# Optimization experiments

Hardware: AMD Instinct MI355X
Metric: run time of the kernel (lower is better)

Reference implementation:

```python
import jax, jax.numpy as jnp
import numpy as np

DEPTH = 10
HID = 48
IN_DIM = 784
OUT_DIM = 10
STEPS = 20
LR = 0.1
BATCH = 65536


def setup_inputs() -> dict:
    key = jax.random.key(0)
    ks = jax.random.split(key, 8)
    x = jax.random.normal(ks[0], (BATCH, IN_DIM), dtype=jnp.float32)
    target = jax.random.randint(ks[1], (BATCH,), 0, OUT_DIM)
    W0 = jax.random.normal(ks[2], (HID, IN_DIM), dtype=jnp.float32) / np.sqrt(IN_DIM)
    b0 = jnp.zeros((HID,), dtype=jnp.float32)
    Wh = jax.random.normal(ks[3], (DEPTH - 1, HID, HID), dtype=jnp.float32) / np.sqrt(HID)
    bh = jnp.zeros((DEPTH - 1, HID), dtype=jnp.float32)
    Wout = jax.random.normal(ks[4], (OUT_DIM, HID), dtype=jnp.float32) / np.sqrt(HID)
    bout = jnp.zeros((OUT_DIM,), dtype=jnp.float32)
    return {"x": x, "target": target, "W0": W0, "b0": b0, "Wh": Wh, "bh": bh, "Wout": Wout, "bout": bout}


def _settle(x, target, W0, b0, Wh, bh, Wout, bout):
    # hidden-layer weights: weights[0] = (W0,b0); weights[i] = (Wh[i-1],bh[i-1]) for 1<=i<DEPTH;
    # output layer weights[DEPTH] = (Wout,bout)
    def hw(i):
        return (W0, b0) if i == 0 else (Wh[i - 1], bh[i - 1])

    # init value nodes with a standard forward pass
    vals = []
    h = x
    for i in range(DEPTH):
        Wi, bi = hw(i)
        h = jax.nn.relu(h @ Wi.T + bi)
        vals.append(h)
    V = jnp.stack(vals, 0)  # (DEPTH, B, HID) = v_1..v_DEPTH
    v_out = jax.nn.one_hot(target, OUT_DIM, dtype=jnp.float32)  # clamped output v_{DEPTH+1}

    def step(V, _):
        vs = [x] + [V[i] for i in range(DEPTH)] + [v_out]
        # prediction errors (computed once per settling step, from pre-step values)
        errors = []
        for i in range(DEPTH):
            Wi, bi = hw(i)
            pre = vs[i] @ Wi.T + bi
            errors.append(vs[i + 1] - jax.nn.relu(pre))
        errors.append(vs[DEPTH + 1] - (vs[DEPTH] @ Wout.T + bout))
        # value-node updates: dE/dv_i = eps_{i-1} - J_i^T eps_i
        new = []
        for i in range(1, DEPTH + 1):
            bu = errors[i - 1]
            if i < DEPTH:
                Wi, bi = hw(i)
                pre = vs[i] @ Wi.T + bi
                td = (errors[i] * (pre > 0).astype(pre.dtype)) @ Wi
            else:
                td = errors[DEPTH] @ Wout
            vi = vs[i] - LR * (bu - td)
            new.append(jnp.clip(vi, -10.0, 10.0))
        return jnp.stack(new, 0), None

    V, _ = jax.lax.scan(step, V, None, length=STEPS)
    return V  # (DEPTH, B, HID): settled hidden value nodes v_1..v_DEPTH


def reference(x, target, W0, b0, Wh, bh, Wout, bout):
    return _settle(x, target, W0, b0, Wh, bh, Wout, bout)
```

## Files before the change

### kernel.cpp

```cpp
#include <hip/hip_runtime.h>
#include <stdint.h>

typedef __attribute__((ext_vector_type(4))) _Float16 half4;
typedef __attribute__((ext_vector_type(2))) _Float16 h2;
typedef __attribute__((ext_vector_type(4))) float f32x4;
typedef __attribute__((ext_vector_type(2))) uint32_t uint2v;
typedef __attribute__((ext_vector_type(2))) short short2v;

#define BLOCK 256
#define MFMA16 __builtin_amdgcn_mfma_f32_16x16x16f16
#define SCHEDB __builtin_amdgcn_sched_barrier
#define PKRTZ  __builtin_amdgcn_cvt_pkrtz

#define TD_OFF    41472
#define BH_OFF    59904
#define LDS_BYTES 61632

extern __shared__ unsigned char smem[];

#define B32H(X) __builtin_bit_cast(uint32_t, (X))
#define H2U(X)  __builtin_bit_cast(h2, (X))

#define PACK4(S0,S1,S2,S3) __extension__({ \
  half4 _b; \
  _b[0] = (_Float16)(S0); _b[1] = (_Float16)(S1); \
  _b[2] = (_Float16)(S2); _b[3] = (_Float16)(S3); \
  _b; })
#define PACKU(S0,S1) __extension__({ \
  h2 _x; _x[0] = (_Float16)(S0); _x[1] = (_Float16)(S1); B32H(_x); })

#define VB(ROW, KS) __extension__({ \
  uint2v _u; _u[0] = (ROW)[2*(KS)]; _u[1] = (ROW)[2*(KS)+1]; \
  __builtin_bit_cast(half4, _u); })

#define TDA(I, ST) ((I) <= 5 \
  ? tdreg[(I) <= 5 ? (I)-1 : 0][ST] \
  : *(const half4*)(smem + TD_OFF + ((I) >= 6 ? (I)-6 : 0)*4608 + (ST)*512 + lane*8))

#define PRED48(SRCU, WOFF, LIDX, P0, P1, P2) do { \
  P0 = *(const f32x4*)(smem + BH_OFF + ((LIDX)*48 +  0)*4 + b*16); \
  P1 = *(const f32x4*)(smem + BH_OFF + ((LIDX)*48 + 16)*4 + b*16); \
  P2 = *(const f32x4*)(smem + BH_OFF + ((LIDX)*48 + 32)*4 + b*16); \
  _Pragma("unroll") \
  for (int _ks = 0; _ks < 3; ++_ks) { \
    half4 _B = VB(SRCU, _ks); \
    half4 _A0 = *(const half4*)(smem + (WOFF) + (0*3+_ks)*512 + lane*8); \
    half4 _A1 = *(const half4*)(smem + (WOFF) + (1*3+_ks)*512 + lane*8); \
    half4 _A2 = *(const half4*)(smem + (WOFF) + (2*3+_ks)*512 + lane*8); \
    P0 = MFMA16(_A0, _B, P0, 0, 0, 0); \
    P1 = MFMA16(_A1, _B, P1, 0, 0, 0); \
    P2 = MFMA16(_A2, _B, P2, 0, 0, 0); \
  } \
} while(0)

#define TD48(MEU, I, T0, T1, T2) do { \
  T0 = (f32x4){0.f,0.f,0.f,0.f}; T1 = T0; T2 = T0; \
  _Pragma("unroll") \
  for (int _ks = 0; _ks < 3; ++_ks) { \
    half4 _B = VB(MEU, _ks); \
    half4 _A0 = TDA(I, 0*3+_ks); \
    half4 _A1 = TDA(I, 1*3+_ks); \
    half4 _A2 = TDA(I, 2*3+_ks); \
    T0 = MFMA16(_A0, _B, T0, 0, 0, 0); \
    T1 = MFMA16(_A1, _B, T1, 0, 0, 0); \
    T2 = MFMA16(_A2, _B, T2, 0, 0, 0); \
  } \
} while(0)

#define PREP2(PLO, PHI, VU32, ERRU, MEU) do { \
  uint32_t _p = B32H(PKRTZ((PLO), (PHI))); \
  uint32_t _sm = __builtin_bit_cast(uint32_t, \
      (short2v)(__builtin_bit_cast(short2v, _p) >> 15)); \
  uint32_t _nsm = ~_sm; \
  uint32_t _rl = _p & _nsm; \
  h2 _e = H2U(VU32) - H2U(_rl); \
  ERRU = B32H(_e); \
  MEU = ERRU & _nsm; \
} while(0)

#define UPD2(TLO, THI, EPKU, VU, ERRU) do { \
  uint32_t _t = B32H(PKRTZ((TLO), (THI))); \
  h2 _d = H2U(EPKU) - H2U(_t); \
  h2 _nv = H2U(VU) - HLR2*_d; \
  _nv = __builtin_elementwise_min(__builtin_elementwise_max(_nv, NCLP2), PCLP2); \
  VU = B32H(_nv); \
  EPKU = ERRU; \
} while(0)

#define LAYER_STEP(I) do { \
  f32x4 _p0, _p1, _p2; \
  PRED48(vhu[(I)-1], ((I)-1)*4608, (I)-1, _p0, _p1, _p2); \
  uint32_t _err[6], _me[6]; \
  PREP2(_p0[0], _p0[1], vhu[I][0], _err[0], _me[0]); \
  PREP2(_p0[2], _p0[3], vhu[I][1], _err[1], _me[1]); \
  PREP2(_p1[0], _p1[1], vhu[I][2], _err[2], _me[2]); \
  PREP2(_p1[2], _p1[3], vhu[I][3], _err[3], _me[3]); \
  PREP2(_p2[0], _p2[1], vhu[I][4], _err[4], _me[4]); \
  PREP2(_p2[2], _p2[3], vhu[I][5], _err[5], _me[5]); \
  f32x4 _t0, _t1, _t2; \
  TD48(_me, I, _t0, _t1, _t2); \
  UPD2(_t0[0], _t0[1], epku[0], vhu[(I)-1][0], _err[0]); \
  UPD2(_t0[2], _t0[3], epku[1], vhu[(I)-1][1], _err[1]); \
  UPD2(_t1[0], _t1[1], epku[2], vhu[(I)-1][2], _err[2]); \
  UPD2(_t1[2], _t1[3], epku[3], vhu[(I)-1][3], _err[3]); \
  UPD2(_t2[0], _t2[1], epku[4], vhu[(I)-1][4], _err[4]); \
  UPD2(_t2[2], _t2[3], epku[5], vhu[(I)-1][5], _err[5]); \
} while(0)

#define FWD(I) do { \
  f32x4 _p0, _p1, _p2; \
  PRED48(vhu[(I)-1], ((I)-1)*4608, (I)-1, _p0, _p1, _p2); \
  vhu[I][0] = PACKU(fmaxf(_p0[0],0.f), fmaxf(_p0[1],0.f)); \
  vhu[I][1] = PACKU(fmaxf(_p0[2],0.f), fmaxf(_p0[3],0.f)); \
  vhu[I][2] = PACKU(fmaxf(_p1[0],0.f), fmaxf(_p1[1],0.f)); \
  vhu[I][3] = PACKU(fmaxf(_p1[2],0.f), fmaxf(_p1[3],0.f)); \
  vhu[I][4] = PACKU(fmaxf(_p2[0],0.f), fmaxf(_p2[1],0.f)); \
  vhu[I][5] = PACKU(fmaxf(_p2[2],0.f), fmaxf(_p2[3],0.f)); \
} while(0)

__global__ __launch_bounds__(BLOCK) __attribute__((amdgpu_waves_per_eu(1, 2)))
void pcnet_kernel(const float* __restrict__ x, const int* __restrict__ target,
                  const float* __restrict__ W0, const float* __restrict__ b0,
                  const float* __restrict__ Wh, const float* __restrict__ bh,
                  const float* __restrict__ Wout, const float* __restrict__ bout,
                  float* __restrict__ out)
{
    const int t = threadIdx.x;
    const int lane = t & 63;
    const int wv = t >> 6;
    const int n = lane & 15;
    const int b = lane >> 4;

    const int bsamp0 = blockIdx.x*64 + wv*16;
    const int samp = bsamp0 + n;

    const h2 HLR2  = (h2)(_Float16)0.1f;
    const h2 PCLP2 = (h2)(_Float16)10.0f;
    const h2 NCLP2 = (h2)(_Float16)(-10.0f);

    f32x4 acc0[3];
    #pragma unroll
    for (int tm = 0; tm < 3; ++tm) acc0[tm] = (f32x4){0.f, 0.f, 0.f, 0.f};

    const float* xrow = x + (size_t)samp*784;
    for (int ch = 0; ch < 7; ++ch) {
        __syncthreads();
        for (int idx = t; idx < 1344; idx += BLOCK) {
            int st = idx >> 6, LB = idx & 63;
            int tm = st / 7, ksl = st - tm*7;
            int row = 16*tm + (LB & 15);
            int col = ch*112 + ksl*16 + 4*(LB >> 4);
            float4 w4 = *(const float4*)(W0 + row*784 + col);
            *(half4*)(smem + (tm*7+ksl)*512 + LB*8) = PACK4(w4.x, w4.y, w4.z, w4.w);
        }
        __syncthreads();
        #pragma unroll
        for (int ksl = 0; ksl < 7; ++ksl) {
            float4 xv = *(const float4*)(xrow + ch*112 + ksl*16 + 4*b);
            half4 xb = PACK4(xv.x, xv.y, xv.z, xv.w);
            #pragma unroll
            for (int tm = 0; tm < 3; ++tm) {
                half4 A = *(const half4*)(smem + (tm*7+ksl)*512 + lane*8);
                acc0[tm] = MFMA16(A, xb, acc0[tm], 0, 0, 0);
            }
        }
    }

    uint32_t vhu[10][6], a0u[6];
    #pragma unroll
    for (int tm = 0; tm < 3; ++tm) {
        float4 bb = *(const float4*)(b0 + 16*tm + 4*b);
        uint32_t lo = PACKU(fmaxf(acc0[tm][0] + bb.x, 0.f), fmaxf(acc0[tm][1] + bb.y, 0.f));
        uint32_t hi = PACKU(fmaxf(acc0[tm][2] + bb.z, 0.f), fmaxf(acc0[tm][3] + bb.w, 0.f));
        a0u[2*tm] = lo;   vhu[0][2*tm] = lo;
        a0u[2*tm+1] = hi; vhu[0][2*tm+1] = hi;
    }
    __syncthreads();

    for (int idx = t; idx < 5184; idx += BLOCK) {
        int L = idx / 576;
        int r2 = idx - L*576;
        int st = r2 >> 6, LB = r2 & 63;
        int tm = st / 3, ks = st - tm*3;
        int m  = 16*tm + (LB & 15);
        int k0 = 16*ks + 4*(LB >> 4);
        float4 w4 = *(const float4*)(Wh + L*2304 + m*48 + k0);
        *(half4*)(smem + L*4608 + st*512 + LB*8) = PACK4(w4.x, w4.y, w4.z, w4.w);
    }
    for (int idx = t; idx < 2304; idx += BLOCK) {
        int Lt = idx / 576;
        int r2 = idx - Lt*576;
        int st = r2 >> 6, LB = r2 & 63;
        int tm = st / 3, ks = st - tm*3;
        int m  = 16*tm + (LB & 15);
        int k0 = 16*ks + 4*(LB >> 4);
        const float* p = Wh + (Lt+5)*2304 + k0*48 + m;
        *(half4*)(smem + TD_OFF + Lt*4608 + st*512 + LB*8) = PACK4(p[0], p[48], p[96], p[144]);
    }
    for (int idx = t; idx < 432; idx += BLOCK)
        *(float*)(smem + BH_OFF + idx*4) = bh[idx];
    __syncthreads();

    half4 tdreg[5][9];
    #pragma unroll
    for (int L = 0; L < 5; ++L)
        #pragma unroll
        for (int st = 0; st < 9; ++st) {
            int tm = st / 3, ks = st - tm*3;
            int m  = 16*tm + (lane & 15);
            int k0 = 16*ks + 4*(lane >> 4);
            const float* p = Wh + L*2304 + k0*48 + m;
            tdreg[L][st] = PACK4(p[0], p[48], p[96], p[144]);
        }
    half4 WP[3], WT[3];
    {
        int c = lane & 15;
        #pragma unroll
        for (int ks = 0; ks < 3; ++ks) {
            if (c < 10) {
                float4 w4 = *(const float4*)(Wout + c*48 + 16*ks + 4*(lane >> 4));
                WP[ks] = PACK4(w4.x, w4.y, w4.z, w4.w);
            } else {
                WP[ks] = PACK4(0.f, 0.f, 0.f, 0.f);
            }
        }
        int c0 = 4*(lane >> 4);
        #pragma unroll
        for (int tm = 0; tm < 3; ++tm) {
            int m = 16*tm + (lane & 15);
            float w0 = (c0+0 < 10) ? Wout[(c0+0)*48 + m] : 0.f;
            float w1 = (c0+1 < 10) ? Wout[(c0+1)*48 + m] : 0.f;
            float w2 = (c0+2 < 10) ? Wout[(c0+2)*48 + m] : 0.f;
            float w3 = (c0+3 < 10) ? Wout[(c0+3)*48 + m] : 0.f;
            WT[tm] = PACK4(w0, w1, w2, w3);
        }
    }
    f32x4 bo4;
    #pragma unroll
    for (int q = 0; q < 4; ++q) bo4[q] = (4*b+q < 10) ? bout[4*b+q] : 0.f;
    const int tg = target[samp];

    FWD(1); FWD(2); FWD(3); FWD(4); FWD(5); FWD(6); FWD(7); FWD(8); FWD(9);
    SCHEDB(0);

    #pragma unroll 1
    for (int s = 0; s < 20; ++s) {
        uint32_t epku[6];
        #pragma unroll
        for (int j = 0; j < 6; ++j)
            epku[j] = B32H(H2U(vhu[0][j]) - H2U(a0u[j]));

        LAYER_STEP(1); LAYER_STEP(2); LAYER_STEP(3);
        SCHEDB(0);
        LAYER_STEP(4); LAYER_STEP(5); LAYER_STEP(6);
        SCHEDB(0);
        LAYER_STEP(7); LAYER_STEP(8); LAYER_STEP(9);
        SCHEDB(0);

        {
            f32x4 accP = bo4;
            #pragma unroll
            for (int ks = 0; ks < 3; ++ks)
                accP = MFMA16(WP[ks], VB(vhu[9], ks), accP, 0, 0, 0);
            int c0 = 4*b;
            float e0 = (c0+0 < 10) ? (((c0+0 == tg) ? 1.f : 0.f) - accP[0]) : 0.f;
            float e1 = (c0+1 < 10) ? (((c0+1 == tg) ? 1.f : 0.f) - accP[1]) : 0.f;
            float e2 = (c0+2 < 10) ? (((c0+2 == tg) ? 1.f : 0.f) - accP[2]) : 0.f;
            float e3 = (c0+3 < 10) ? (((c0+3 == tg) ? 1.f : 0.f) - accP[3]) : 0.f;
            uint32_t eBu[2];
            eBu[0] = B32H(PKRTZ(e0, e1));
            eBu[1] = B32H(PKRTZ(e2, e3));
            half4 eB = VB(eBu, 0);
            #pragma unroll
            for (int tm = 0; tm < 3; ++tm) {
                f32x4 a2 = {0.f, 0.f, 0.f, 0.f};
                a2 = MFMA16(WT[tm], eB, a2, 0, 0, 0);
                uint32_t dummy_err = 0;
                uint32_t e_lo = epku[2*tm], e_hi = epku[2*tm+1];
                {
                    uint32_t _t = B32H(PKRTZ(a2[0], a2[1]));
                    h2 _d = H2U(e_lo) - H2U(_t);
                    h2 _nv = H2U(vhu[9][2*tm]) - HLR2*_d;
                    _nv = __builtin_elementwise_min(__builtin_elementwise_max(_nv, NCLP2), PCLP2);
                    vhu[9][2*tm] = B32H(_nv);
                }
                {
                    uint32_t _t = B32H(PKRTZ(a2[2], a2[3]));
                    h2 _d = H2U(e_hi) - H2U(_t);
                    h2 _nv = H2U(vhu[9][2*tm+1]) - HLR2*_d;
                    _nv = __builtin_elementwise_min(__builtin_elementwise_max(_nv, NCLP2), PCLP2);
                    vhu[9][2*tm+1] = B32H(_nv);
                }
                (void)dummy_err;
            }
            SCHEDB(0);
        }
    }

    #pragma unroll
    for (int L2 = 0; L2 < 10; ++L2) {
        #pragma unroll
        for (int tt = 0; tt < 3; ++tt) {
            h2 lo = H2U(vhu[L2][2*tt]);
            h2 hi = H2U(vhu[L2][2*tt+1]);
            f32x4 w4 = { (float)lo[0], (float)lo[1], (float)hi[0], (float)hi[1] };
            *(f32x4*)(out + (size_t)L2*65536*48 + (size_t)samp*48 + tt*16 + 4*b) = w4;
        }
    }
}

extern "C" void kernel_launch(void* const* d_in, const int* in_sizes, int n_in,
                              void* d_out, int out_size, void* d_ws, size_t ws_size,
                              hipStream_t stream) {
    const float* x      = (const float*)d_in[0];
    const int*   target = (const int*)d_in[1];
    const float* W0     = (const float*)d_in[2];
    const float* b0     = (const float*)d_in[3];
    const float* Wh     = (const float*)d_in[4];
    const float* bh     = (const float*)d_in[5];
    const float* Wout   = (const float*)d_in[6];
    const float* bout   = (const float*)d_in[7];
    float* out = (float*)d_out;

    hipFuncSetAttribute((const void*)pcnet_kernel,
                        hipFuncAttributeMaxDynamicSharedMemorySize, LDS_BYTES);

    dim3 grid(65536/64);
    dim3 block(BLOCK);
    pcnet_kernel<<<grid, block, LDS_BYTES, stream>>>(x, target, W0, b0, Wh, bh, Wout, bout, out);
}
```

Before: 297.6 us.

## Software-pipeline next layer's prediction MFMAs with current layer's top-down pass

Restructures the settling loop so that each layer step issues the next layer's prediction MFMAs (which depend only on pre-update values) before the current layer's top-down MFMAs and updates. This gives the scheduler independent MFMA chains to interleave and hide MFMA latency. The sched_barriers between layer groups are removed. ReLU is now computed with a packed half max instead of sign-mask AND, and the code keeps three extra accumulator vectors live, which raises register pressure.

```diff
diff --git a/kernel.cpp b/kernel.cpp
--- a/kernel.cpp
+++ b/kernel.cpp
@@ -71,11 +71,10 @@
   uint32_t _p = B32H(PKRTZ((PLO), (PHI))); \
   uint32_t _sm = __builtin_bit_cast(uint32_t, \
       (short2v)(__builtin_bit_cast(short2v, _p) >> 15)); \
-  uint32_t _nsm = ~_sm; \
-  uint32_t _rl = _p & _nsm; \
-  h2 _e = H2U(VU32) - H2U(_rl); \
+  h2 _rl = __builtin_elementwise_max(H2U(_p), ZH2); \
+  h2 _e = H2U(VU32) - _rl; \
   ERRU = B32H(_e); \
-  MEU = ERRU & _nsm; \
+  MEU = ~_sm & ERRU; \
 } while(0)
 
 #define UPD2(TLO, THI, EPKU, VU, ERRU) do { \
@@ -87,16 +86,16 @@
   EPKU = ERRU; \
 } while(0)
 
-#define LAYER_STEP(I) do { \
-  f32x4 _p0, _p1, _p2; \
-  PRED48(vhu[(I)-1], ((I)-1)*4608, (I)-1, _p0, _p1, _p2); \
+#define STEP_P(I, HASNEXT) do { \
   uint32_t _err[6], _me[6]; \
-  PREP2(_p0[0], _p0[1], vhu[I][0], _err[0], _me[0]); \
-  PREP2(_p0[2], _p0[3], vhu[I][1], _err[1], _me[1]); \
-  PREP2(_p1[0], _p1[1], vhu[I][2], _err[2], _me[2]); \
-  PREP2(_p1[2], _p1[3], vhu[I][3], _err[3], _me[3]); \
-  PREP2(_p2[0], _p2[1], vhu[I][4], _err[4], _me[4]); \
-  PREP2(_p2[2], _p2[3], vhu[I][5], _err[5], _me[5]); \
+  PREP2(P0[0], P0[1], vhu[I][0], _err[0], _me[0]); \
+  PREP2(P0[2], P0[3], vhu[I][1], _err[1], _me[1]); \
+  PREP2(P1[0], P1[1], vhu[I][2], _err[2], _me[2]); \
+  PREP2(P1[2], P1[3], vhu[I][3], _err[3], _me[3]); \
+  PREP2(P2[0], P2[1], vhu[I][4], _err[4], _me[4]); \
+  PREP2(P2[2], P2[3], vhu[I][5], _err[5], _me[5]); \
+  f32x4 _n0 = P0, _n1 = P1, _n2 = P2; \
+  if (HASNEXT) PRED48(vhu[I], (I)*4608, I, _n0, _n1, _n2); \
   f32x4 _t0, _t1, _t2; \
   TD48(_me, I, _t0, _t1, _t2); \
   UPD2(_t0[0], _t0[1], epku[0], vhu[(I)-1][0], _err[0]); \
@@ -105,6 +104,7 @@
   UPD2(_t1[2], _t1[3], epku[3], vhu[(I)-1][3], _err[3]); \
   UPD2(_t2[0], _t2[1], epku[4], vhu[(I)-1][4], _err[4]); \
   UPD2(_t2[2], _t2[3], epku[5], vhu[(I)-1][5], _err[5]); \
+  P0 = _n0; P1 = _n1; P2 = _n2; \
 } while(0)
 
 #define FWD(I) do { \
@@ -137,6 +137,7 @@
     const h2 HLR2  = (h2)(_Float16)0.1f;
     const h2 PCLP2 = (h2)(_Float16)10.0f;
     const h2 NCLP2 = (h2)(_Float16)(-10.0f);
+    const h2 ZH2   = (h2)(_Float16)0.0f;
 
     f32x4 acc0[3];
     #pragma unroll
@@ -250,12 +251,11 @@
         for (int j = 0; j < 6; ++j)
             epku[j] = B32H(H2U(vhu[0][j]) - H2U(a0u[j]));
 
-        LAYER_STEP(1); LAYER_STEP(2); LAYER_STEP(3);
-        SCHEDB(0);
-        LAYER_STEP(4); LAYER_STEP(5); LAYER_STEP(6);
-        SCHEDB(0);
-        LAYER_STEP(7); LAYER_STEP(8); LAYER_STEP(9);
-        SCHEDB(0);
+        f32x4 P0, P1, P2;
+        PRED48(vhu[0], 0*4608, 0, P0, P1, P2);
+        STEP_P(1, 1); STEP_P(2, 1); STEP_P(3, 1); STEP_P(4, 1);
+        STEP_P(5, 1); STEP_P(6, 1); STEP_P(7, 1); STEP_P(8, 1);
+        STEP_P(9, 0);
 
         {
             f32x4 accP = bo4;
@@ -275,25 +275,21 @@
             for (int tm = 0; tm < 3; ++tm) {
                 f32x4 a2 = {0.f, 0.f, 0.f, 0.f};
                 a2 = MFMA16(WT[tm], eB, a2, 0, 0, 0);
-                uint32_t dummy_err = 0;
-                uint32_t e_lo = epku[2*tm], e_hi = epku[2*tm+1];
                 {
                     uint32_t _t = B32H(PKRTZ(a2[0], a2[1]));
-                    h2 _d = H2U(e_lo) - H2U(_t);
+                    h2 _d = H2U(epku[2*tm]) - H2U(_t);
                     h2 _nv = H2U(vhu[9][2*tm]) - HLR2*_d;
                     _nv = __builtin_elementwise_min(__builtin_elementwise_max(_nv, NCLP2), PCLP2);
                     vhu[9][2*tm] = B32H(_nv);
                 }
                 {
                     uint32_t _t = B32H(PKRTZ(a2[2], a2[3]));
-                    h2 _d = H2U(e_hi) - H2U(_t);
+                    h2 _d = H2U(epku[2*tm+1]) - H2U(_t);
                     h2 _nv = H2U(vhu[9][2*tm+1]) - HLR2*_d;
                     _nv = __builtin_elementwise_min(__builtin_elementwise_max(_nv, NCLP2), PCLP2);
                     vhu[9][2*tm+1] = B32H(_nv);
                 }
-                (void)dummy_err;
             }
-            SCHEDB(0);
         }
     }
 
```

Result: slower. 586.6 us (+97.1%).
